# Kernel tuning notes

Measured on AMD Instinct MI355X. Metric: run time of the kernel, lower is better.

Reference implementation:

```python
import jax, jax.numpy as jnp
import numpy as np

H, W, S = 480, 1024, 32
MULT_THRESH, ADD_THRESH = 0.01, 0.1


def setup_inputs() -> dict:
    key = jax.random.key(0)
    k1, k2 = jax.random.split(key)
    flows_f = jax.random.normal(k1, (1, S, 2, H, W), jnp.float32)
    noise = jax.random.normal(k2, (1, S, 2, H, W), jnp.float32)
    # near-inverse backward flow so the fwd-bwd consistency check passes for many points
    flows_b = -flows_f + 0.05 * noise
    return {"flows_f": flows_f, "flows_b": flows_b, "margin": 10, "sample_step": 4}


def bilinear_sample(im, x, y):
    # im: (C,H,W); x,y: (N,) float pixel coords -> (C,N). Matches torch bilinear_sample2d
    # (weights from unclipped coords, gather indices clipped to the image).
    C, Hh, Ww = im.shape
    x0 = jnp.floor(x); y0 = jnp.floor(y)
    wx1 = x - x0; wx0 = 1.0 - wx1
    wy1 = y - y0; wy0 = 1.0 - wy1
    x0i = jnp.clip(x0.astype(jnp.int32), 0, Ww - 1)
    x1i = jnp.clip(x0i + 1, 0, Ww - 1)
    y0i = jnp.clip(y0.astype(jnp.int32), 0, Hh - 1)
    y1i = jnp.clip(y0i + 1, 0, Hh - 1)
    g = lambda yi, xi: im[:, yi, xi]  # (C,N)
    return (g(y0i, x0i) * (wy0 * wx0) + g(y0i, x1i) * (wy0 * wx1)
            + g(y1i, x0i) * (wy1 * wx0) + g(y1i, x1i) * (wy1 * wx1))


def _forward(ff, fb, margin, sample_step):
    # ff, fb: (S, 2, H, W) forward / backward flows (batch squeezed, B=1)
    gy = jnp.arange(margin, H - margin + 1, sample_step, dtype=jnp.float32)
    gx = jnp.arange(margin, W - margin + 1, sample_step, dtype=jnp.float32)
    YY, XX = jnp.meshgrid(gy, gx, indexing='ij')
    ys_g = YY.reshape(-1); xs_g = XX.reshape(-1)          # (G,) base sampling grid
    G = xs_g.shape[0]
    N = 2 * H * W // (sample_step ** 2)                   # trajectory slot capacity
    R = min(N, G)                                         # max births per step (static)

    by, bx = jnp.meshgrid(jnp.arange(H, dtype=jnp.float32),
                          jnp.arange(W, dtype=jnp.float32), indexing='ij')

    def prune(flow_f, flow_b):
        # fwd-bwd consistency mask 'on': (H,W) in {0,1}
        xt = (bx + flow_f[0]).reshape(-1)
        yt = (by + flow_f[1]).reshape(-1)
        fbw = bilinear_sample(flow_b, xt, yt).reshape(2, H, W)  # backwarped bwd flow
        diff = jnp.sqrt(jnp.sum((flow_f + fbw) ** 2, axis=0))
        mag = 0.5 * (jnp.sqrt(jnp.sum(flow_f ** 2, axis=0)) + jnp.sqrt(jnp.sum(fbw ** 2, axis=0)))
        return (diff <= MULT_THRESH * mag + ADD_THRESH).astype(jnp.float32)

    X = jnp.zeros((S, N), jnp.float32)
    Y = jnp.zeros((S, N), jnp.float32)
    Start = -jnp.ones((N,), jnp.float32)
    X = X.at[0, :G].set(xs_g)
    Y = Y.at[0, :G].set(ys_g)
    Start = Start.at[:G].set(0.0)

    def step(carry, inp):
        X, Y, Start = carry
        flow_f, flow_b, s = inp
        on = prune(flow_f, flow_b)                         # (H,W)
        active = Start >= 0.0                              # (N,) live-slot mask (replaces where(Start>=0))
        xs_o = X[s]; ys_o = Y[s]
        uv = bilinear_sample(flow_f, xs_o, ys_o)           # (2,N) flow at current points
        xs_t = xs_o + uv[0]; ys_t = ys_o + uv[1]
        fb_ok = bilinear_sample(on[None], xs_o, ys_o)[0] > 0.5
        marg = ((xs_t > margin) & (ys_t > margin) &
                (xs_t < W - margin) & (ys_t < H - margin))
        choose = active & marg & fb_ok
        # scatter surviving points into row s+1 (row starts as zeros, matching init)
        X = X.at[s + 1].set(jnp.where(choose, xs_t, 0.0))
        Y = Y.at[s + 1].set(jnp.where(choose, ys_t, 0.0))
        Start = jnp.where(active & ~choose, -1.0, Start)   # terminated slots freed
        # occupancy map of surviving targets, dilated by 5x5 ones-conv (== maxpool on binary)
        oy = jnp.where(choose, ys_t, jnp.float32(H)).astype(jnp.int32)
        ox = jnp.where(choose, xs_t, jnp.float32(W)).astype(jnp.int32)
        occ = jnp.zeros((H, W), jnp.float32).at[oy, ox].set(1.0, mode='drop')
        occ = jax.lax.reduce_window(occ, 0.0, jax.lax.max, (5, 5), (1, 1), 'SAME')
        map_occ = bilinear_sample(occ[None], xs_g, ys_g)[0]
        free_cand = (1.0 - map_occ) == 1.0                 # (G,) unoccupied grid points
        # compaction without dynamic shapes: stable-sort free-first, keep original order
        cand_order = jnp.argsort(~free_cand, stable=True)  # free candidates first
        num_cand = jnp.sum(free_cand)
        free_slot = Start < 0.0
        slot_order = jnp.argsort(~free_slot, stable=True)  # free slots first
        num_free = jnp.sum(free_slot)
        m = jnp.minimum(num_cand, num_free)
        r = jnp.arange(R)
        tgt = jnp.where(r < m, slot_order[:R], N)          # index N -> dropped
        X = X.at[s + 1, tgt].set(xs_g[cand_order[:R]], mode='drop')
        Y = Y.at[s + 1, tgt].set(ys_g[cand_order[:R]], mode='drop')
        Start = Start.at[tgt].set((s + 1).astype(jnp.float32), mode='drop')
        return (X, Y, Start), None

    steps = jnp.arange(S - 1)
    (X, Y, Start), _ = jax.lax.scan(step, (X, Y, Start), (ff[:-1], fb[:-1], steps))
    return jnp.stack([X, Y]), Start


def reference(flows_f, flows_b, margin, sample_step):
    # Returns dense trajectory buffers XY: (2, S, N) and final Start: (N,)
    # (the ragged python-list trajectory extraction is a host-side post-process).
    return _forward(flows_f[0], flows_b[0], margin, sample_step)
```

## Files before the change

kernel.cpp:

```cpp
#include <hip/hip_runtime.h>
#include <cstdint>

#define HH 480
#define WW 1024
#define SS 32
#define HW (HH*WW)
#define MARGIN 10
#define STEP 4
#define GYC 116
#define GXC 252
#define GG (GYC*GXC)
#define NSLOT (2*HH*WW/(STEP*STEP))
#define NBLK (NSLOT/256)
#define NWAVE (NSLOT/64)
#define CW ((GG+63)/64)
#define CWP 512
#define OCCB (CW*64)
#define FS8 32
#define FP8 (256*FS8)
#define CPB 122

__device__ __forceinline__ unsigned int aload(const unsigned int* p) {
  return __hip_atomic_load(p, __ATOMIC_RELAXED, __HIP_MEMORY_SCOPE_AGENT);
}
__device__ __forceinline__ void astore(unsigned int* p, unsigned int v) {
  __hip_atomic_store(p, v, __ATOMIC_RELAXED, __HIP_MEMORY_SCOPE_AGENT);
}
__device__ __forceinline__ unsigned long long aload64(const unsigned long long* p) {
  return __hip_atomic_load(p, __ATOMIC_RELAXED, __HIP_MEMORY_SCOPE_AGENT);
}
__device__ __forceinline__ void astore64(unsigned long long* p, unsigned long long v) {
  __hip_atomic_store(p, v, __ATOMIC_RELAXED, __HIP_MEMORY_SCOPE_AGENT);
}
__device__ __forceinline__ void astore8(unsigned char* p, unsigned char v) {
  __hip_atomic_store(p, v, __ATOMIC_RELAXED, __HIP_MEMORY_SCOPE_AGENT);
}

__device__ __forceinline__ int clampi(int v, int lo, int hi) {
  return v < lo ? lo : (v > hi ? hi : v);
}

__global__ __launch_bounds__(256) void k_init(unsigned long long* __restrict__ flags,
                                              unsigned int* __restrict__ occ32)
{
  int idx = blockIdx.x * 256 + threadIdx.x;
  if (idx < (2 * OCCB / 4)) occ32[idx] = 0u;
  if (idx < 256) {
    unsigned long long v = (idx < NBLK) ? 0ull : (0x7FFFFFFFull << 32);
    flags[idx * FS8] = v;
    flags[FP8 + idx * FS8] = v;
  }
}

__device__ __forceinline__ void barrier_ps4(unsigned long long* flagbase, int epoch,
                                            int myblk, int* ps4, const int* wcnt)
{
  __syncthreads();
  if (threadIdx.x == 0) {
    unsigned cpack = (unsigned)wcnt[0] | ((unsigned)wcnt[1] << 8)
                   | ((unsigned)wcnt[2] << 16) | ((unsigned)wcnt[3] << 24);
    astore64(&flagbase[myblk * FS8],
             ((unsigned long long)(unsigned)epoch << 32) | (unsigned long long)cpack);
  }
  if (threadIdx.x < 64) {
    const int lane = threadIdx.x;
    unsigned long long v0, v1, v2, v3;
    for (;;) {
      v0 = aload64(&flagbase[(lane      ) * FS8]);
      v1 = aload64(&flagbase[(lane +  64) * FS8]);
      v2 = aload64(&flagbase[(lane + 128) * FS8]);
      v3 = aload64(&flagbase[(lane + 192) * FS8]);
      unsigned m0 = (unsigned)(v0 >> 32), m1 = (unsigned)(v1 >> 32);
      unsigned m2 = (unsigned)(v2 >> 32), m3 = (unsigned)(v3 >> 32);
      unsigned mn = m0 < m1 ? m0 : m1;
      unsigned mn2 = m2 < m3 ? m2 : m3;
      mn = mn < mn2 ? mn : mn2;
      for (int o = 32; o > 0; o >>= 1) {
        unsigned t = (unsigned)__shfl_xor((int)mn, o, 64);
        mn = mn < t ? mn : t;
      }
      if ((int)mn >= epoch) break;
      __builtin_amdgcn_s_sleep(1);
    }
    auto up = [](unsigned long long f) -> unsigned long long {
      unsigned c = (unsigned)f;
      return (unsigned long long)(c & 0xFFu)
           | ((unsigned long long)((c >>  8) & 0xFFu) << 16)
           | ((unsigned long long)((c >> 16) & 0xFFu) << 32)
           | ((unsigned long long)((c >> 24) & 0xFFu) << 48);
    };
    unsigned long long u0 = up(v0), u1 = up(v1), u2 = up(v2), u3 = up(v3);
    unsigned long long F = u0 + u1 + u2 + u3;
    unsigned long long P = (lane       < myblk ? u0 : 0ull)
                         + (lane +  64 < myblk ? u1 : 0ull)
                         + (lane + 128 < myblk ? u2 : 0ull)
                         + (lane + 192 < myblk ? u3 : 0ull);
    for (int o = 32; o > 0; o >>= 1) {
      unsigned flo = (unsigned)F, fhi = (unsigned)(F >> 32);
      unsigned plo = (unsigned)P, phi = (unsigned)(P >> 32);
      unsigned flo2 = (unsigned)__shfl_xor((int)flo, o, 64);
      unsigned fhi2 = (unsigned)__shfl_xor((int)fhi, o, 64);
      unsigned plo2 = (unsigned)__shfl_xor((int)plo, o, 64);
      unsigned phi2 = (unsigned)__shfl_xor((int)phi, o, 64);
      F += ((unsigned long long)fhi2 << 32) | flo2;
      P += ((unsigned long long)phi2 << 32) | plo2;
    }
    if (lane == 0) {
      int f0 = (int)(F & 0xFFFF), f1 = (int)((F >> 16) & 0xFFFF), f2 = (int)((F >> 32) & 0xFFFF);
      int p0 = (int)(P & 0xFFFF), p1 = (int)((P >> 16) & 0xFFFF);
      int p2 = (int)((P >> 32) & 0xFFFF), p3 = (int)((P >> 48) & 0xFFFF);
      ps4[0] = p0;
      ps4[1] = f0 + p1;
      ps4[2] = f0 + f1 + p2;
      ps4[3] = f0 + f1 + f2 + p3;
    }
  }
  __syncthreads();
}

struct Bil {
  int x0i, x1i, y0i, y1i;
  int i00, i01, i10, i11;
  float w00, w01, w10, w11;
};

__device__ __forceinline__ Bil mkbil(float xs, float ys) {
#pragma clang fp contract(off)
  float x0 = floorf(xs), y0 = floorf(ys);
  float wx1 = xs - x0, wx0 = 1.0f - wx1;
  float wy1 = ys - y0, wy0 = 1.0f - wy1;
  Bil b;
  b.x0i = clampi((int)x0, 0, WW - 1);
  b.x1i = b.x0i + 1 > WW - 1 ? WW - 1 : b.x0i + 1;
  b.y0i = clampi((int)y0, 0, HH - 1);
  b.y1i = b.y0i + 1 > HH - 1 ? HH - 1 : b.y0i + 1;
  b.i00 = b.y0i * WW + b.x0i; b.i01 = b.y0i * WW + b.x1i;
  b.i10 = b.y1i * WW + b.x0i; b.i11 = b.y1i * WW + b.x1i;
  b.w00 = wy0 * wx0; b.w01 = wy0 * wx1;
  b.w10 = wy1 * wx0; b.w11 = wy1 * wx1;
  return b;
}

__device__ __forceinline__ float prune_val(float fx, float fy,
    float c00a, float c01a, float c10a, float c11a,
    float c00b, float c01b, float c10b, float c11b, const Bil& t)
{
#pragma clang fp contract(off)
  float bw0 = ((c00a * t.w00 + c01a * t.w01) + c10a * t.w10) + c11a * t.w11;
  float bw1 = ((c00b * t.w00 + c01b * t.w01) + c10b * t.w10) + c11b * t.w11;
  float t0 = fx + bw0, t1 = fy + bw1;
  float diff = sqrtf(t0 * t0 + t1 * t1);
  float magf = sqrtf(fx * fx + fy * fy);
  float magb = sqrtf(bw0 * bw0 + bw1 * bw1);
  float mag = 0.5f * (magf + magb);
  return (diff <= 0.01f * mag + 0.1f) ? 1.0f : 0.0f;
}

__device__ __forceinline__ unsigned long long make_intadv(
    int pix, int piy, float fx, float fy, const float* __restrict__ bks)
{
#pragma clang fp contract(off)
  float xt = (float)pix + fx, yt = (float)piy + fy;
  Bil Bt = mkbil(xt, yt);
  const float* b0p = bks;
  const float* b1p = bks + HW;
  float o = prune_val(fx, fy,
                      b0p[Bt.i00], b0p[Bt.i01], b0p[Bt.i10], b0p[Bt.i11],
                      b1p[Bt.i00], b1p[Bt.i01], b1p[Bt.i10], b1p[Bt.i11], Bt);
  bool marg = (xt > (float)MARGIN) && (yt > (float)MARGIN) &&
              (xt < (float)(WW - MARGIN)) && (yt < (float)(HH - MARGIN));
  bool ch = marg && (o > 0.5f);
  unsigned lo = __float_as_uint(ch ? xt : 0.0f);
  unsigned hi = __float_as_uint(ch ? yt : -1.0f);
  return ((unsigned long long)hi << 32) | (unsigned long long)lo;
}

__global__ __launch_bounds__(256, 1) void k_steps(
    const float* __restrict__ ff, const float* __restrict__ fbk,
    float* __restrict__ X, float* __restrict__ Y, float* __restrict__ Start,
    unsigned char* __restrict__ occ, unsigned long long* __restrict__ flags,
    unsigned long long* __restrict__ intadv)
{
#pragma clang fp contract(off)
  const int b = blockIdx.x;
  const int lane = threadIdx.x & 63;
  const int wv = threadIdx.x >> 6;
  const int slot = ((wv * NBLK + b) << 6) | lane;
  const unsigned long long ltmask = (1ull << lane) - 1ull;

  __shared__ unsigned long long wds[CWP];
  __shared__ unsigned int pref[CWP];
  __shared__ int wsum[4];
  __shared__ int wcnt[2][4];
  __shared__ int ps4[4];

  float x = 0.f, y = 0.f, st = -1.f;
  int mode = 0;
  float pf0 = 0.f, pf1 = 0.f, pf2 = 0.f, pf3 = 0.f;
  float pf4 = 0.f, pf5 = 0.f, pf6 = 0.f, pf7 = 0.f;
  float pb[32];
  float pxt = 0.f, pyt = 0.f;
  bool  pmarg = false;
  unsigned long long pa64 = (unsigned long long)0xBF800000u << 32;

  const int pj = threadIdx.x >> 1;
  const int pcell = b * CPB + pj;
  const bool prod = ((threadIdx.x & 1) == 0) && (pj < CPB) && (pcell < GG);
  int pix = 0, piy = 0, pp = 0;
  float fNx = 0.f, fNy = 0.f;
  float fCx = 0.f, fCy = 0.f;
  float bC0 = 0.f, bC1 = 0.f, bC2 = 0.f, bC3 = 0.f;
  float bC4 = 0.f, bC5 = 0.f, bC6 = 0.f, bC7 = 0.f;

  if (slot < GG) {
    int ii = slot / GXC, jj = slot - ii * GXC;
    int ix = MARGIN + STEP * jj, iy = MARGIN + STEP * ii;
    x = (float)ix; y = (float)iy;
    st = 0.f; mode = 2;
    int p0_ = iy * WW + ix;
    float f0x = ff[p0_], f0y = ff[HW + p0_];
    pa64 = make_intadv(ix, iy, f0x, f0y, fbk);
  }
  X[slot] = x; Y[slot] = y;

  if (prod) {
    int ii = pcell / GXC, jj = pcell - ii * GXC;
    pix = MARGIN + STEP * jj; piy = MARGIN + STEP * ii;
    pp = piy * WW + pix;
    float f1x = ff[(size_t)1 * 2 * HW + pp], f1y = ff[(size_t)1 * 2 * HW + HW + pp];
    float f2x = ff[(size_t)2 * 2 * HW + pp], f2y = ff[(size_t)2 * 2 * HW + HW + pp];
    float f3x = ff[(size_t)3 * 2 * HW + pp], f3y = ff[(size_t)3 * 2 * HW + HW + pp];
    fNx = ff[(size_t)4 * 2 * HW + pp];       fNy = ff[(size_t)4 * 2 * HW + HW + pp];
    astore64(&intadv[(size_t)1 * GG + pcell],
             make_intadv(pix, piy, f1x, f1y, fbk + (size_t)1 * 2 * HW));
    astore64(&intadv[(size_t)2 * GG + pcell],
             make_intadv(pix, piy, f2x, f2y, fbk + (size_t)2 * 2 * HW));
    {
      float xt = (float)pix + f3x, yt = (float)piy + f3y;
      Bil Bt = mkbil(xt, yt);
      const float* bb0 = fbk + (size_t)3 * 2 * HW;
      const float* bb1 = bb0 + HW;
      bC0 = bb0[Bt.i00]; bC1 = bb0[Bt.i01]; bC2 = bb0[Bt.i10]; bC3 = bb0[Bt.i11];
      bC4 = bb1[Bt.i00]; bC5 = bb1[Bt.i01]; bC6 = bb1[Bt.i10]; bC7 = bb1[Bt.i11];
      fCx = f3x; fCy = f3y;
    }
  }

#define ISSUE_TAP(tt, TXI, TYI, FX, FY) do { \
    Bil Bt = mkbil((float)P.TXI + (FX), (float)P.TYI + (FY)); \
    pb[(tt)*8+0] = b0n[Bt.i00]; pb[(tt)*8+1] = b0n[Bt.i01]; \
    pb[(tt)*8+2] = b0n[Bt.i10]; pb[(tt)*8+3] = b0n[Bt.i11]; \
    pb[(tt)*8+4] = b1n[Bt.i00]; pb[(tt)*8+5] = b1n[Bt.i01]; \
    pb[(tt)*8+6] = b1n[Bt.i10]; pb[(tt)*8+7] = b1n[Bt.i11]; \
  } while (0)

#define PRUNE_TAP(tt, TXI, TYI, FX, FY, OUT) do { \
    Bil Bt = mkbil((float)P.TXI + (FX), (float)P.TYI + (FY)); \
    OUT = prune_val((FX), (FY), \
                    pb[(tt)*8+0], pb[(tt)*8+1], pb[(tt)*8+2], pb[(tt)*8+3], \
                    pb[(tt)*8+4], pb[(tt)*8+5], pb[(tt)*8+6], pb[(tt)*8+7], Bt); \
  } while (0)

  for (int s = 0; s < SS - 1; ++s) {
    const float* f0n = ff + (size_t)(s + 1) * 2 * HW;
    const float* f1n = f0n + HW;
    const unsigned char tag = (unsigned char)(s + 1);
    unsigned char* occw = occ + (((s + 1) & 1) ? OCCB : 0);

    bool moved = false;
    if (mode == 1) {
      Bil P = mkbil(x, y);
      float o0, o1, o2, o3;
      PRUNE_TAP(0, x0i, y0i, pf0, pf4, o0);
      PRUNE_TAP(1, x1i, y0i, pf1, pf5, o1);
      PRUNE_TAP(2, x0i, y1i, pf2, pf6, o2);
      PRUNE_TAP(3, x1i, y1i, pf3, pf7, o3);
      float fbv = ((o0 * P.w00 + o1 * P.w01) + o2 * P.w10) + o3 * P.w11;
      if (pmarg && fbv > 0.5f) {
        x = pxt; y = pyt;
        Bil Pn = mkbil(x, y);
        pf0 = f0n[Pn.i00]; pf1 = f0n[Pn.i01]; pf2 = f0n[Pn.i10]; pf3 = f0n[Pn.i11];
        pf4 = f1n[Pn.i00]; pf5 = f1n[Pn.i01]; pf6 = f1n[Pn.i10]; pf7 = f1n[Pn.i11];
        moved = true;
      } else { st = -1.f; x = 0.f; y = 0.f; mode = 0; }
    } else if (mode == 2) {
      float axt = __uint_as_float((unsigned)pa64);
      float ayt = __uint_as_float((unsigned)(pa64 >> 32));
      if (ayt >= 0.0f) {
        x = axt; y = ayt; mode = 1;
        Bil Pn = mkbil(x, y);
        pf0 = f0n[Pn.i00]; pf1 = f0n[Pn.i01]; pf2 = f0n[Pn.i10]; pf3 = f0n[Pn.i11];
        pf4 = f1n[Pn.i00]; pf5 = f1n[Pn.i01]; pf6 = f1n[Pn.i10]; pf7 = f1n[Pn.i11];
        moved = true;
      } else { st = -1.f; x = 0.f; y = 0.f; mode = 0; }
    }
    if (moved) {
      int oy = (int)y, ox = (int)x;
      int i0 = ((oy - (MARGIN + 2) + 4099) >> 2) - 1024;
      int i1 = ((oy - (MARGIN - 2) + 4096) >> 2) - 1024;
      int j0 = ((ox - (MARGIN + 2) + 4099) >> 2) - 1024;
      int j1 = ((ox - (MARGIN - 2) + 4096) >> 2) - 1024;
      if (i0 < 0) i0 = 0; if (i1 > GYC - 1) i1 = GYC - 1;
      if (j0 < 0) j0 = 0; if (j1 > GXC - 1) j1 = GXC - 1;
      for (int i = i0; i <= i1; ++i)
        for (int j = j0; j <= j1; ++j)
          astore8(&occw[i * GXC + j], tag);
    }
    unsigned long long smask = __ballot(st < 0.0f);
    if (lane == 0) wcnt[s & 1][wv] = (int)__popcll(smask);

    barrier_ps4(flags + (s & 1) * FP8, s + 1, b, ps4, wcnt[s & 1]);
    int ps = ps4[wv];

    unsigned long long cv[16];
    {
      const unsigned long long* occ64 =
          (const unsigned long long*)(occ + (((s + 1) & 1) ? OCCB : 0));
      int t = threadIdx.x;
#pragma unroll
      for (int r = 0; r < 16; ++r) {
        int j = t + 256 * r;
        cv[r] = (j < GG / 8) ? aload64(&occ64[j]) : 0ull;
      }
    }
    if (mode == 1 && s < SS - 2) {
      Bil P = mkbil(x, y);
      float u_ = ((pf0 * P.w00 + pf1 * P.w01) + pf2 * P.w10) + pf3 * P.w11;
      float v_ = ((pf4 * P.w00 + pf5 * P.w01) + pf6 * P.w10) + pf7 * P.w11;
      pxt = x + u_; pyt = y + v_;
      pmarg = (pxt > (float)MARGIN) && (pyt > (float)MARGIN) &&
              (pxt < (float)(WW - MARGIN)) && (pyt < (float)(HH - MARGIN));
      const float* b0n = fbk + (size_t)(s + 1) * 2 * HW;
      const float* b1n = b0n + HW;
      ISSUE_TAP(0, x0i, y0i, pf0, pf4);
      ISSUE_TAP(1, x1i, y0i, pf1, pf5);
      ISSUE_TAP(2, x0i, y1i, pf2, pf6);
      ISSUE_TAP(3, x1i, y1i, pf3, pf7);
    }
    if (prod) {
      if (s <= SS - 5) {
        float xt = (float)pix + fCx, yt = (float)piy + fCy;
        Bil Bt = mkbil(xt, yt);
        float o = prune_val(fCx, fCy, bC0, bC1, bC2, bC3, bC4, bC5, bC6, bC7, Bt);
        bool marg = (xt > (float)MARGIN) && (yt > (float)MARGIN) &&
                    (xt < (float)(WW - MARGIN)) && (yt < (float)(HH - MARGIN));
        bool ch = marg && (o > 0.5f);
        unsigned lo = __float_as_uint(ch ? xt : 0.0f);
        unsigned hi = __float_as_uint(ch ? yt : -1.0f);
        astore64(&intadv[(size_t)(s + 3) * GG + pcell],
                 ((unsigned long long)hi << 32) | (unsigned long long)lo);
      }
      if (s <= SS - 6) {
        float xt = (float)pix + fNx, yt = (float)piy + fNy;
        Bil Bt = mkbil(xt, yt);
        const float* bb0 = fbk + (size_t)(s + 4) * 2 * HW;
        const float* bb1 = bb0 + HW;
        bC0 = bb0[Bt.i00]; bC1 = bb0[Bt.i01]; bC2 = bb0[Bt.i10]; bC3 = bb0[Bt.i11];
        bC4 = bb1[Bt.i00]; bC5 = bb1[Bt.i01]; bC6 = bb1[Bt.i10]; bC7 = bb1[Bt.i11];
        fCx = fNx; fCy = fNy;
      }
      if (s <= SS - 7) {
        const float* fp_ = ff + (size_t)(s + 5) * 2 * HW;
        fNx = fp_[pp]; fNy = fp_[HW + pp];
      }
    }
    {
      unsigned char* nb = (unsigned char*)wds;
      const unsigned long long tr = 0x0101010101010101ull * (unsigned long long)tag;
      int t = threadIdx.x;
#pragma unroll
      for (int r = 0; r < 16; ++r) {
        int j = t + 256 * r;
        unsigned long long xx = cv[r] ^ tr;
        unsigned long long t1 = (xx & 0x7F7F7F7F7F7F7F7Full) + 0x7F7F7F7F7F7F7F7Full;
        unsigned long long nz = ((t1 | xx) >> 7) & 0x0101010101010101ull;
        unsigned char byte = (unsigned char)((nz * 0x0102040810204080ull) >> 56);
        nb[j] = (j < GG / 8) ? byte : (unsigned char)0;
      }
    }
    __syncthreads();
    {
      int t = threadIdx.x;
      int e0 = 2 * t, e1 = 2 * t + 1;
      unsigned long long m0 = wds[e0];
      unsigned long long m1 = wds[e1];
      int p0 = __popcll(m0), p1 = __popcll(m1);
      int v = p0 + p1;
      for (int o = 1; o < 64; o <<= 1) {
        int uu = __shfl_up(v, o, 64);
        if (lane >= o) v += uu;
      }
      if (lane == 63) wsum[wv] = v;
      __syncthreads();
      int base = 0;
      for (int j2 = 0; j2 < wv; ++j2) base += wsum[j2];
      pref[e0] = (unsigned int)(base + v - p1);
      pref[e1] = (unsigned int)(base + v);
      __syncthreads();
    }
    int tc = (int)pref[CWP - 1];

    if (st < 0.0f) {
      int r = ps + (int)__popcll(smask & ltmask);
      if (r < tc) {
        int k = 0;
        for (int bb = 256; bb >= 1; bb >>= 1) {
          int nk = k + bb;
          if (nk <= CWP - 1 && (int)pref[nk - 1] <= r) k = nk;
        }
        int j = r - (k ? (int)pref[k - 1] : 0);
        unsigned long long m = wds[k];
        int lo = 0;
        for (int bb = 32; bb >= 1; bb >>= 1) {
          int nb2 = lo + bb;
          unsigned long long mask = (nb2 >= 64) ? ~0ull : ((1ull << nb2) - 1ull);
          if (__popcll(m & mask) <= j) lo = nb2;
        }
        int g = k * 64 + lo;
        int ii = g / GXC, jj = g - ii * GXC;
        x = (float)(MARGIN + STEP * jj);
        y = (float)(MARGIN + STEP * ii);
        st = (float)(s + 1);
        mode = 2;
        if (s < SS - 2)
          pa64 = aload64(&intadv[(size_t)(s + 1) * GG + g]);
      }
    }
    X[(size_t)(s + 1) * NSLOT + slot] = x;
    Y[(size_t)(s + 1) * NSLOT + slot] = y;
  }

#undef ISSUE_TAP
#undef PRUNE_TAP

  Start[slot] = st;
}

extern "C" void kernel_launch(void* const* d_in, const int* in_sizes, int n_in,
                              void* d_out, int out_size, void* d_ws, size_t ws_size,
                              hipStream_t stream) {
  const float* ff  = (const float*)d_in[0];
  const float* fbk = (const float*)d_in[1];

  float* X     = (float*)d_out;
  float* Y     = X + (size_t)SS * NSLOT;
  float* Start = Y + (size_t)SS * NSLOT;

  unsigned long long* flags  = (unsigned long long*)d_ws;
  unsigned char*      occ    = (unsigned char*)(flags + 2 * FP8);
  unsigned long long* intadv = (unsigned long long*)(occ + 2 * OCCB);

  k_init<<<58, 256, 0, stream>>>(flags, (unsigned int*)occ);

  k_steps<<<NBLK, 256, 0, stream>>>(ff, fbk, X, Y, Start, occ, flags, intadv);
}
```

Measured before the change: 428.6 us.

## Split the grid barrier into arrive/wait phases and pack the flag array

```diff
diff --git a/kernel.cpp b/kernel.cpp
--- a/kernel.cpp
+++ b/kernel.cpp
@@ -16,8 +16,7 @@
 #define CW ((GG+63)/64)
 #define CWP 512
 #define OCCB (CW*64)
-#define FS8 32
-#define FP8 (256*FS8)
+#define FPW 256
 #define CPB 122
 
 __device__ __forceinline__ unsigned int aload(const unsigned int* p) {
@@ -47,75 +46,9 @@
   if (idx < (2 * OCCB / 4)) occ32[idx] = 0u;
   if (idx < 256) {
     unsigned long long v = (idx < NBLK) ? 0ull : (0x7FFFFFFFull << 32);
-    flags[idx * FS8] = v;
-    flags[FP8 + idx * FS8] = v;
+    flags[idx] = v;
+    flags[FPW + idx] = v;
   }
-}
-
-__device__ __forceinline__ void barrier_ps4(unsigned long long* flagbase, int epoch,
-                                            int myblk, int* ps4, const int* wcnt)
-{
-  __syncthreads();
-  if (threadIdx.x == 0) {
-    unsigned cpack = (unsigned)wcnt[0] | ((unsigned)wcnt[1] << 8)
-                   | ((unsigned)wcnt[2] << 16) | ((unsigned)wcnt[3] << 24);
-    astore64(&flagbase[myblk * FS8],
-             ((unsigned long long)(unsigned)epoch << 32) | (unsigned long long)cpack);
-  }
-  if (threadIdx.x < 64) {
-    const int lane = threadIdx.x;
-    unsigned long long v0, v1, v2, v3;
-    for (;;) {
-      v0 = aload64(&flagbase[(lane      ) * FS8]);
-      v1 = aload64(&flagbase[(lane +  64) * FS8]);
-      v2 = aload64(&flagbase[(lane + 128) * FS8]);
-      v3 = aload64(&flagbase[(lane + 192) * FS8]);
-      unsigned m0 = (unsigned)(v0 >> 32), m1 = (unsigned)(v1 >> 32);
-      unsigned m2 = (unsigned)(v2 >> 32), m3 = (unsigned)(v3 >> 32);
-      unsigned mn = m0 < m1 ? m0 : m1;
-      unsigned mn2 = m2 < m3 ? m2 : m3;
-      mn = mn < mn2 ? mn : mn2;
-      for (int o = 32; o > 0; o >>= 1) {
-        unsigned t = (unsigned)__shfl_xor((int)mn, o, 64);
-        mn = mn < t ? mn : t;
-      }
-      if ((int)mn >= epoch) break;
-      __builtin_amdgcn_s_sleep(1);
-    }
-    auto up = [](unsigned long long f) -> unsigned long long {
-      unsigned c = (unsigned)f;
-      return (unsigned long long)(c & 0xFFu)
-           | ((unsigned long long)((c >>  8) & 0xFFu) << 16)
-           | ((unsigned long long)((c >> 16) & 0xFFu) << 32)
-           | ((unsigned long long)((c >> 24) & 0xFFu) << 48);
-    };
-    unsigned long long u0 = up(v0), u1 = up(v1), u2 = up(v2), u3 = up(v3);
-    unsigned long long F = u0 + u1 + u2 + u3;
-    unsigned long long P = (lane       < myblk ? u0 : 0ull)
-                         + (lane +  64 < myblk ? u1 : 0ull)
-                         + (lane + 128 < myblk ? u2 : 0ull)
-                         + (lane + 192 < myblk ? u3 : 0ull);
-    for (int o = 32; o > 0; o >>= 1) {
-      unsigned flo = (unsigned)F, fhi = (unsigned)(F >> 32);
-      unsigned plo = (unsigned)P, phi = (unsigned)(P >> 32);
-      unsigned flo2 = (unsigned)__shfl_xor((int)flo, o, 64);
-      unsigned fhi2 = (unsigned)__shfl_xor((int)fhi, o, 64);
-      unsigned plo2 = (unsigned)__shfl_xor((int)plo, o, 64);
-      unsigned phi2 = (unsigned)__shfl_xor((int)phi, o, 64);
-      F += ((unsigned long long)fhi2 << 32) | flo2;
-      P += ((unsigned long long)phi2 << 32) | plo2;
-    }
-    if (lane == 0) {
-      int f0 = (int)(F & 0xFFFF), f1 = (int)((F >> 16) & 0xFFFF), f2 = (int)((F >> 32) & 0xFFFF);
-      int p0 = (int)(P & 0xFFFF), p1 = (int)((P >> 16) & 0xFFFF);
-      int p2 = (int)((P >> 32) & 0xFFFF), p3 = (int)((P >> 48) & 0xFFFF);
-      ps4[0] = p0;
-      ps4[1] = f0 + p1;
-      ps4[2] = f0 + f1 + p2;
-      ps4[3] = f0 + f1 + f2 + p3;
-    }
-  }
-  __syncthreads();
 }
 
 struct Bil {
@@ -309,20 +242,17 @@
     unsigned long long smask = __ballot(st < 0.0f);
     if (lane == 0) wcnt[s & 1][wv] = (int)__popcll(smask);
 
-    barrier_ps4(flags + (s & 1) * FP8, s + 1, b, ps4, wcnt[s & 1]);
-    int ps = ps4[wv];
-
-    unsigned long long cv[16];
-    {
-      const unsigned long long* occ64 =
-          (const unsigned long long*)(occ + (((s + 1) & 1) ? OCCB : 0));
-      int t = threadIdx.x;
-#pragma unroll
-      for (int r = 0; r < 16; ++r) {
-        int j = t + 256 * r;
-        cv[r] = (j < GG / 8) ? aload64(&occ64[j]) : 0ull;
-      }
-    }
+    unsigned long long* fb = flags + (s & 1) * FPW;
+    const int epoch = s + 1;
+    __syncthreads();
+    if (threadIdx.x == 0) {
+      const int* wc = wcnt[s & 1];
+      unsigned cpack = (unsigned)wc[0] | ((unsigned)wc[1] << 8)
+                     | ((unsigned)wc[2] << 16) | ((unsigned)wc[3] << 24);
+      astore64(&fb[b],
+               ((unsigned long long)(unsigned)epoch << 32) | (unsigned long long)cpack);
+    }
+
     if (mode == 1 && s < SS - 2) {
       Bil P = mkbil(x, y);
       float u_ = ((pf0 * P.w00 + pf1 * P.w01) + pf2 * P.w10) + pf3 * P.w11;
@@ -362,6 +292,73 @@
       if (s <= SS - 7) {
         const float* fp_ = ff + (size_t)(s + 5) * 2 * HW;
         fNx = fp_[pp]; fNy = fp_[HW + pp];
+      }
+    }
+
+    if (threadIdx.x < 64) {
+      unsigned long long v0, v1, v2, v3;
+      for (;;) {
+        v0 = aload64(&fb[lane      ]);
+        v1 = aload64(&fb[lane +  64]);
+        v2 = aload64(&fb[lane + 128]);
+        v3 = aload64(&fb[lane + 192]);
+        unsigned m0 = (unsigned)(v0 >> 32), m1 = (unsigned)(v1 >> 32);
+        unsigned m2 = (unsigned)(v2 >> 32), m3 = (unsigned)(v3 >> 32);
+        unsigned mn = m0 < m1 ? m0 : m1;
+        unsigned mn2 = m2 < m3 ? m2 : m3;
+        mn = mn < mn2 ? mn : mn2;
+        for (int o = 32; o > 0; o >>= 1) {
+          unsigned t = (unsigned)__shfl_xor((int)mn, o, 64);
+          mn = mn < t ? mn : t;
+        }
+        if ((int)mn >= epoch) break;
+        __builtin_amdgcn_s_sleep(1);
+      }
+      auto up = [](unsigned long long f) -> unsigned long long {
+        unsigned c = (unsigned)f;
+        return (unsigned long long)(c & 0xFFu)
+             | ((unsigned long long)((c >>  8) & 0xFFu) << 16)
+             | ((unsigned long long)((c >> 16) & 0xFFu) << 32)
+             | ((unsigned long long)((c >> 24) & 0xFFu) << 48);
+      };
+      unsigned long long u0 = up(v0), u1 = up(v1), u2 = up(v2), u3 = up(v3);
+      unsigned long long F = u0 + u1 + u2 + u3;
+      unsigned long long Pp = (lane       < b ? u0 : 0ull)
+                            + (lane +  64 < b ? u1 : 0ull)
+                            + (lane + 128 < b ? u2 : 0ull)
+                            + (lane + 192 < b ? u3 : 0ull);
+      for (int o = 32; o > 0; o >>= 1) {
+        unsigned flo = (unsigned)F, fhi = (unsigned)(F >> 32);
+        unsigned plo = (unsigned)Pp, phi = (unsigned)(Pp >> 32);
+        unsigned flo2 = (unsigned)__shfl_xor((int)flo, o, 64);
+        unsigned fhi2 = (unsigned)__shfl_xor((int)fhi, o, 64);
+        unsigned plo2 = (unsigned)__shfl_xor((int)plo, o, 64);
+        unsigned phi2 = (unsigned)__shfl_xor((int)phi, o, 64);
+        F  += ((unsigned long long)fhi2 << 32) | flo2;
+        Pp += ((unsigned long long)phi2 << 32) | plo2;
+      }
+      if (lane == 0) {
+        int f0 = (int)(F & 0xFFFF), f1 = (int)((F >> 16) & 0xFFFF), f2 = (int)((F >> 32) & 0xFFFF);
+        int p0 = (int)(Pp & 0xFFFF), p1 = (int)((Pp >> 16) & 0xFFFF);
+        int p2 = (int)((Pp >> 32) & 0xFFFF), p3 = (int)((Pp >> 48) & 0xFFFF);
+        ps4[0] = p0;
+        ps4[1] = f0 + p1;
+        ps4[2] = f0 + f1 + p2;
+        ps4[3] = f0 + f1 + f2 + p3;
+      }
+    }
+    __syncthreads();
+    int ps = ps4[wv];
+
+    unsigned long long cv[16];
+    {
+      const unsigned long long* occ64 =
+          (const unsigned long long*)(occ + (((s + 1) & 1) ? OCCB : 0));
+      int t = threadIdx.x;
+#pragma unroll
+      for (int r = 0; r < 16; ++r) {
+        int j = t + 256 * r;
+        cv[r] = (j < GG / 8) ? aload64(&occ64[j]) : 0ull;
       }
     }
     {
@@ -447,7 +444,7 @@
   float* Start = Y + (size_t)SS * NSLOT;
 
   unsigned long long* flags  = (unsigned long long*)d_ws;
-  unsigned char*      occ    = (unsigned char*)(flags + 2 * FP8);
+  unsigned char*      occ    = (unsigned char*)(flags + 2 * FPW);
   unsigned long long* intadv = (unsigned long long*)(occ + 2 * OCCB);
 
   k_init<<<58, 256, 0, stream>>>(flags, (unsigned int*)occ);
```

New measurement: 417.5 us. 2.6% less time.
